# Optimization experiments

Hardware: AMD Instinct MI355X
Metric: run time of the kernel (lower is better)

The kernel has to match this reference:

```python
import jax, jax.numpy as jnp
import numpy as np

P_ORDER = 3  # cubic B-spline (spline_order in the torch module)


def _make_knots(degree, lo, hi, order):
    # mirrors Transformation.__init__ knot construction
    d = (hi - lo) / (degree - 1)
    return np.linspace(lo - order * d, hi + order * d, degree + 2 * order).astype(np.float32)


def setup_inputs() -> dict:
    key = jax.random.key(0)
    N, V, degree = 500000, 8, 40
    M = degree + P_ORDER - 1  # 42 coefficients per variable
    k1, k2 = jax.random.split(key)
    # data inside the spline range [-3, 3]
    x = jax.random.uniform(k1, (N, V), minval=-2.9, maxval=2.9, dtype=jnp.float32)
    # unrestricted params in the style of compute_starting_values (inverse softplus of increments)
    base = np.linspace(-3.0, 3.0, M).astype(np.float32)
    raw = base.copy()
    raw[1:] = np.log(np.exp(base[1:] - base[:-1]) - 1.0)
    raw_params = jnp.asarray(np.tile(raw[:, None], (1, V)))
    raw_params = raw_params + 0.01 * jax.random.normal(k2, raw_params.shape, dtype=jnp.float32)
    knots = jnp.asarray(np.stack([_make_knots(degree, -3.0, 3.0, P_ORDER) for _ in range(V)], axis=1))  # [46, V]
    return {"x": x, "raw_params": raw_params, "knots": knots}


def _deboor(x, t, c, p):
    # vectorized deBoor evaluation: x [N], knots t [K], coeffs c [K-p-1]
    K = t.shape[0]
    k = jnp.clip(jnp.searchsorted(t, x, side='right') - 1, p, K - p - 2)  # knot span per point
    j = jnp.arange(p + 1)
    d = c[k[:, None] - p + j]  # [N, p+1] local coefficients (gather)
    for r in range(1, p + 1):
        for jj in range(p, r - 1, -1):
            tl = t[jj + k - p]
            tr = t[jj + 1 + k - r]
            alpha = (x - tl) / (tr - tl)
            d = d.at[:, jj].set((1.0 - alpha) * d[:, jj - 1] + alpha * d[:, jj])
    return d[:, p]


def _eval_var(xv, tv, cv):
    p = P_ORDER
    M = cv.shape[0]
    y = _deboor(xv, tv, cv, p)
    # derivative spline: degree p-1, coeffs from first differences of c
    q = p * (cv[1:] - cv[:-1]) / (tv[p + 1:p + M] - tv[1:M])
    dy = _deboor(xv, tv[1:-1], q, p - 1)
    return y, dy


def reference(x, raw_params, knots):
    # restrict_parameters with monotonically_increasing: softplus increments + cumsum
    incr = jnp.concatenate([raw_params[:1], jax.nn.softplus(raw_params[1:])], axis=0)
    c = jnp.cumsum(incr, axis=0)  # [M, V] monotone coefficients
    y, dy = jax.vmap(_eval_var, in_axes=(1, 1, 1), out_axes=1)(x, knots, c)
    log_d = jnp.log(dy)  # log-determinant contribution of the monotone transform
    return y, log_d
```

## Files before the change

### kernel.cpp

```cpp
#include <hip/hip_runtime.h>
#include <cmath>

#define NV    8
#define NM    42
#define NK    46
#define TOT_C (NM * NV)

__global__ void prep_kernel(const float* __restrict__ raw,
                            const float* __restrict__ knots,
                            float* __restrict__ c,
                            float* __restrict__ q) {
    __shared__ float s[TOT_C];
    int tid = threadIdx.x;
    if (tid < TOT_C) {
        float r = raw[tid];
        float inc;
        if (tid < NV) {
            inc = r;
        } else {
            inc = (r > 0.f) ? (r + log1pf(expf(-r))) : log1pf(expf(r));
        }
        s[tid] = inc;
    }
    __syncthreads();
    for (int off = 1; off < NM; off <<= 1) {
        float val = 0.f;
        if (tid < TOT_C) {
            int j = tid >> 3;
            val = s[tid] + ((j >= off) ? s[tid - off * NV] : 0.f);
        }
        __syncthreads();
        if (tid < TOT_C) s[tid] = val;
        __syncthreads();
    }
    if (tid < TOT_C) {
        int j = tid >> 3, v = tid & 7;
        float cj = s[tid];
        c[tid] = cj;
        float qj = 0.f;
        if (j < NM - 1) {
            float cn = s[tid + NV];
            qj = 3.f * (cn - cj) / (knots[(j + 4) * NV + v] - knots[(j + 1) * NV + v]);
        }
        q[tid] = qj;
    }
}

__global__ __launch_bounds__(256) void eval_kernel(
        const float* __restrict__ x,
        const float* __restrict__ knots,
        const float* __restrict__ c,
        const float* __restrict__ q,
        float* __restrict__ y_out,
        float* __restrict__ ld_out,
        int total) {
    __shared__ float sc[TOT_C];
    __shared__ float sq[TOT_C];
    __shared__ float st0[NV];
    __shared__ float sinvd[NV];
    int tid = threadIdx.x;
    for (int j = tid; j < TOT_C; j += 256) {
        sc[j] = c[j];
        sq[j] = q[j];
    }
    if (tid < NV) {
        float t0 = knots[tid];
        st0[tid] = t0;
        sinvd[tid] = 1.0f / (knots[NV + tid] - t0);
    }
    __syncthreads();

    int i = blockIdx.x * 256 + tid;
    if (i >= total) return;
    int v = i & (NV - 1);
    float xv = x[i];

    float f = (xv - st0[v]) * sinvd[v];
    int k = (int)floorf(f);
    k = min(max(k, 3), NK - 5);
    float u = f - (float)k;

    int base = (k - 3) * NV + v;
    float c0 = sc[base], c1 = sc[base + NV], c2 = sc[base + 2 * NV], c3 = sc[base + 3 * NV];
    float q0 = sq[base], q1 = sq[base + NV], q2 = sq[base + 2 * NV];

    float omu = 1.f - u;
    float u2 = u * u,  o2 = omu * omu;
    float u3 = u2 * u, o3 = o2 * omu;
    const float k6 = 0.16666666666f;
    float B0 = o3 * k6;
    float B3 = u3 * k6;
    float B1 = (3.f * u3 - 6.f * u2 + 4.f) * k6;
    float B2 = 1.f - B0 - B1 - B3;
    float yv = fmaf(B0, c0, fmaf(B1, c1, fmaf(B2, c2, B3 * c3)));

    float w0 = 0.5f * o2, w2 = 0.5f * u2, w1 = 1.f - w0 - w2;
    float dy = fmaf(w0, q0, fmaf(w1, q1, w2 * q2));

    y_out[i]  = yv;
    ld_out[i] = __logf(dy);
}

extern "C" void kernel_launch(void* const* d_in, const int* in_sizes, int n_in,
                              void* d_out, int out_size, void* d_ws, size_t ws_size,
                              hipStream_t stream) {
    const float* x     = (const float*)d_in[0];
    const float* raw   = (const float*)d_in[1];
    const float* knots = (const float*)d_in[2];

    float* c = (float*)d_ws;
    float* q = c + TOT_C;

    int total = in_sizes[0];
    float* y_out  = (float*)d_out;
    float* ld_out = y_out + total;

    prep_kernel<<<1, 384, 0, stream>>>(raw, knots, c, q);
    int blocks = (total + 255) / 256;
    eval_kernel<<<blocks, 256, 0, stream>>>(x, knots, c, q, y_out, ld_out, total);
}
```

Before: 86.05 us.

## Vectorize eval kernel to 4 elements per thread with transposed LDS tables

Each thread now handles four consecutive inputs using 128-bit loads and nontemporal 128-bit stores, which cuts the block count and the per-block coefficient preload to a quarter. The coefficient and derivative tables in shared memory are transposed to a per-variable layout with stride 48, so each point's four coefficients are contiguous. The aim is fewer memory instructions and less LDS preload per element, in exchange for more registers per thread and fewer threads to hide latency.

```diff
diff --git a/kernel.cpp b/kernel.cpp
--- a/kernel.cpp
+++ b/kernel.cpp
@@ -5,6 +5,9 @@
 #define NM    42
 #define NK    46
 #define TOT_C (NM * NV)
+#define LDS_STRIDE 48
+
+typedef float f32x4 __attribute__((ext_vector_type(4)));
 
 __global__ void prep_kernel(const float* __restrict__ raw,
                             const float* __restrict__ knots,
@@ -46,43 +49,19 @@
     }
 }
 
-__global__ __launch_bounds__(256) void eval_kernel(
-        const float* __restrict__ x,
-        const float* __restrict__ knots,
-        const float* __restrict__ c,
-        const float* __restrict__ q,
-        float* __restrict__ y_out,
-        float* __restrict__ ld_out,
-        int total) {
-    __shared__ float sc[TOT_C];
-    __shared__ float sq[TOT_C];
-    __shared__ float st0[NV];
-    __shared__ float sinvd[NV];
-    int tid = threadIdx.x;
-    for (int j = tid; j < TOT_C; j += 256) {
-        sc[j] = c[j];
-        sq[j] = q[j];
-    }
-    if (tid < NV) {
-        float t0 = knots[tid];
-        st0[tid] = t0;
-        sinvd[tid] = 1.0f / (knots[NV + tid] - t0);
-    }
-    __syncthreads();
-
-    int i = blockIdx.x * 256 + tid;
-    if (i >= total) return;
-    int v = i & (NV - 1);
-    float xv = x[i];
-
+__device__ __forceinline__ void eval_one(float xv, int v,
+                                         const float* __restrict__ sc,
+                                         const float* __restrict__ sq,
+                                         const float* __restrict__ st0,
+                                         const float* __restrict__ sinvd,
+                                         float& yv, float& ldv) {
     float f = (xv - st0[v]) * sinvd[v];
     int k = (int)floorf(f);
     k = min(max(k, 3), NK - 5);
     float u = f - (float)k;
-
-    int base = (k - 3) * NV + v;
-    float c0 = sc[base], c1 = sc[base + NV], c2 = sc[base + 2 * NV], c3 = sc[base + 3 * NV];
-    float q0 = sq[base], q1 = sq[base + NV], q2 = sq[base + 2 * NV];
+    int base = v * LDS_STRIDE + (k - 3);
+    float c0 = sc[base], c1 = sc[base + 1], c2 = sc[base + 2], c3 = sc[base + 3];
+    float q0 = sq[base], q1 = sq[base + 1], q2 = sq[base + 2];
 
     float omu = 1.f - u;
     float u2 = u * u,  o2 = omu * omu;
@@ -92,13 +71,59 @@
     float B3 = u3 * k6;
     float B1 = (3.f * u3 - 6.f * u2 + 4.f) * k6;
     float B2 = 1.f - B0 - B1 - B3;
-    float yv = fmaf(B0, c0, fmaf(B1, c1, fmaf(B2, c2, B3 * c3)));
+    yv = fmaf(B0, c0, fmaf(B1, c1, fmaf(B2, c2, B3 * c3)));
 
     float w0 = 0.5f * o2, w2 = 0.5f * u2, w1 = 1.f - w0 - w2;
-    float dy = fmaf(w0, q0, fmaf(w1, q1, w2 * q2));
+    ldv = __logf(fmaf(w0, q0, fmaf(w1, q1, w2 * q2)));
+}
 
-    y_out[i]  = yv;
-    ld_out[i] = __logf(dy);
+__global__ __launch_bounds__(256) void eval_kernel(
+        const float* __restrict__ x,
+        const float* __restrict__ knots,
+        const float* __restrict__ c,
+        const float* __restrict__ q,
+        float* __restrict__ y_out,
+        float* __restrict__ ld_out,
+        int total) {
+    __shared__ float sc[NV * LDS_STRIDE];
+    __shared__ float sq[NV * LDS_STRIDE];
+    __shared__ float st0[NV];
+    __shared__ float sinvd[NV];
+    int tid = threadIdx.x;
+    for (int idx = tid; idx < TOT_C; idx += 256) {
+        int j = idx >> 3, v = idx & 7;
+        sc[v * LDS_STRIDE + j] = c[idx];
+        sq[v * LDS_STRIDE + j] = q[idx];
+    }
+    if (tid < NV) {
+        float t0 = knots[tid];
+        st0[tid] = t0;
+        sinvd[tid] = 1.0f / (knots[NV + tid] - t0);
+    }
+    __syncthreads();
+
+    int t = blockIdx.x * 256 + tid;
+    int i0 = t * 4;
+    if (i0 + 3 < total) {
+        f32x4 xv = *(const f32x4*)(x + i0);
+        int v0 = i0 & (NV - 1);
+        float y0, y1, y2, y3, l0, l1, l2, l3;
+        eval_one(xv.x, v0,     sc, sq, st0, sinvd, y0, l0);
+        eval_one(xv.y, v0 + 1, sc, sq, st0, sinvd, y1, l1);
+        eval_one(xv.z, v0 + 2, sc, sq, st0, sinvd, y2, l2);
+        eval_one(xv.w, v0 + 3, sc, sq, st0, sinvd, y3, l3);
+        f32x4 yv = {y0, y1, y2, y3};
+        f32x4 lv = {l0, l1, l2, l3};
+        __builtin_nontemporal_store(yv, (f32x4*)(y_out + i0));
+        __builtin_nontemporal_store(lv, (f32x4*)(ld_out + i0));
+    } else {
+        for (int i = i0; i < total; ++i) {
+            float yv, lv;
+            eval_one(x[i], i & (NV - 1), sc, sq, st0, sinvd, yv, lv);
+            y_out[i]  = yv;
+            ld_out[i] = lv;
+        }
+    }
 }
 
 extern "C" void kernel_launch(void* const* d_in, const int* in_sizes, int n_in,
@@ -116,6 +141,7 @@
     float* ld_out = y_out + total;
 
     prep_kernel<<<1, 384, 0, stream>>>(raw, knots, c, q);
-    int blocks = (total + 255) / 256;
+    int nthreads = (total + 3) / 4;
+    int blocks = (nthreads + 255) / 256;
     eval_kernel<<<blocks, 256, 0, stream>>>(x, knots, c, q, y_out, ld_out, total);
 }
```

Measured after the change: 82.00 us, median of 2. 4.7% less time.
